# Performance work log

Hardware: AMD Instinct MI355X
Metric: run time of the kernel (lower is better)

## Reference

```python
import math
import jax, jax.numpy as jnp
import numpy as np

N_WIRES = 12
N_LAYERS = 3
BATCH = 2048
DIM = 2 ** N_WIRES


def _apply_1q(psi, U, wire):
    # psi: (B, 2^n) complex; U: (2,2) or (B,2,2)
    B = psi.shape[0]
    left = 2 ** wire
    psi = psi.reshape(B, left, 2, -1)
    if U.ndim == 3:
        psi = jnp.einsum('bij,bajc->baic', U, psi)
    else:
        psi = jnp.einsum('ij,bajc->baic', U, psi)
    return psi.reshape(B, -1)


def _apply_cnot(psi, wire):
    # CNOT on (control=wire, target=wire+1), adjacent wires
    B = psi.shape[0]
    left = 2 ** wire
    psi = psi.reshape(B, left, 2, 2, -1)
    flipped = psi[:, :, 1, ::-1, :][:, :, None]   # control=1 branch, target flipped
    psi = jnp.concatenate([psi[:, :, 0:1], flipped], axis=2)
    return psi.reshape(B, -1)


def _ry(theta):
    # RY(t) = [[cos t/2, -sin t/2],[sin t/2, cos t/2]]; theta: () or (B,)
    c = jnp.cos(theta / 2)
    s = jnp.sin(theta / 2)
    U = jnp.stack([jnp.stack([c, -s], -1), jnp.stack([s, c], -1)], -2)
    return U.astype(jnp.complex64)


def _rz(theta):
    # RZ(t) = diag(e^{-it/2}, e^{it/2}); theta scalar
    em = jnp.exp(-0.5j * theta.astype(jnp.complex64))
    ep = jnp.exp(0.5j * theta.astype(jnp.complex64))
    e00 = jnp.array([[1, 0], [0, 0]], dtype=jnp.complex64)
    e11 = jnp.array([[0, 0], [0, 1]], dtype=jnp.complex64)
    return e00 * em + e11 * ep


def _measure_z(psi):
    # <Z_w> for every wire; psi: (B, 2^n)
    B = psi.shape[0]
    p = jnp.abs(psi) ** 2
    outs = []
    for w in range(N_WIRES):
        pr = p.reshape(B, 2 ** w, 2, -1)
        outs.append(pr[:, :, 0].sum((1, 2)) - pr[:, :, 1].sum((1, 2)))
    return jnp.stack(outs, axis=-1)  # (B, n_wires)


def _forward(x, W1, b1, ry_theta, rz_theta, W2, b2):
    feat = x @ W1.T + b1                      # (B, n_wires)
    angles = jnp.tanh(feat) * math.pi         # encoding angles
    B = x.shape[0]
    psi = jnp.zeros((B, DIM), dtype=jnp.complex64).at[:, 0].set(1.0)
    # data encoding: per-sample RY on each wire
    for w in range(N_WIRES):
        psi = _apply_1q(psi, _ry(angles[:, w]), w)
    # variational layers with SHARED ry/rz params (module reuse in torch code)
    Ury = _ry(ry_theta)
    Urz = _rz(rz_theta)
    for _ in range(N_LAYERS):
        for w in range(N_WIRES):
            psi = _apply_1q(psi, Ury, w)
            psi = _apply_1q(psi, Urz, w)
        for w in range(N_WIRES - 1):
            psi = _apply_cnot(psi, w)
    z = _measure_z(psi)                        # (B, n_wires) real
    return z @ W2.T + b2                       # (B, 10) logits


def setup_inputs() -> dict:
    key = jax.random.key(0)
    ks = jax.random.split(key, 7)
    return {
        'x': jax.random.normal(ks[0], (BATCH, 784), dtype=jnp.float32),
        'W1': jax.random.normal(ks[1], (N_WIRES, 784), dtype=jnp.float32) * 0.03,
        'b1': jnp.zeros((N_WIRES,), dtype=jnp.float32),
        'ry_theta': jax.random.uniform(ks[2], (), dtype=jnp.float32) * 2 * math.pi,
        'rz_theta': jax.random.uniform(ks[3], (), dtype=jnp.float32) * 2 * math.pi,
        'W2': jax.random.normal(ks[4], (10, N_WIRES), dtype=jnp.float32) * 0.2,
        'b2': jnp.zeros((10,), dtype=jnp.float32),
    }


def reference(x, W1, b1, ry_theta, rz_theta, W2, b2):
    return _forward(x, W1, b1, ry_theta, rz_theta, W2, b2)
```

## Files before the change

### kernel.cpp

```cpp
#include <hip/hip_runtime.h>
#include <math.h>

#define NW   12
#define DIM  4096
#define TPB  256

typedef float v2f __attribute__((ext_vector_type(2)));

template<int CTRL>
__device__ __forceinline__ float fdpp(float v) {
    union { float f; int i; } u, w;
    u.f = v;
    w.i = __builtin_amdgcn_update_dpp(0, u.i, CTRL, 0xF, 0xF, false);
    return w.f;
}

template<int B>
__device__ __forceinline__ void ry_reg(v2f* r, float c, v2f vps, v2f vms) {
#pragma unroll
    for (int p = 0; p < 8; ++p) {
        const int i0 = ((p >> B) << (B + 1)) | (p & ((1 << B) - 1));
        const int i1 = i0 | (1 << B);
        const v2f a = r[i0], b = r[i1];
        r[i0] = __builtin_elementwise_fma(vms, b, a * c);
        r[i1] = __builtin_elementwise_fma(vps, a, b * c);
    }
}

template<int CTRL>
__device__ __forceinline__ void ry_dpp(v2f* r, float c, v2f vsp) {
#pragma unroll
    for (int k = 0; k < 16; ++k) {
        const v2f p = { fdpp<CTRL>(r[k].x), fdpp<CTRL>(r[k].y) };
        r[k] = __builtin_elementwise_fma(vsp, p, r[k] * c);
    }
}

__device__ __forceinline__ void ry_xor4(v2f* r, float c, v2f vsp) {
#pragma unroll
    for (int k = 0; k < 16; ++k) {
        const v2f p = { fdpp<0x141>(fdpp<0x1B>(r[k].x)),
                        fdpp<0x141>(fdpp<0x1B>(r[k].y)) };
        r[k] = __builtin_elementwise_fma(vsp, p, r[k] * c);
    }
}

__global__ __launch_bounds__(TPB, 4)
void qmnist_kernel(const float* __restrict__ x,  const float* __restrict__ W1,
                   const float* __restrict__ b1, const float* __restrict__ ryp,
                   const float* __restrict__ rzp, const float* __restrict__ W2,
                   const float* __restrict__ b2, float* __restrict__ out) {
    __shared__ v2f psi[DIM];
    float* smf  = (float*)psi;
    float* wred = smf;
    float* encc = smf + 48;
    float* encs = smf + 60;
    float* zfin = smf + 72;

    const int tid  = threadIdx.x;
    const int blk  = blockIdx.x;
    const int lane = tid & 63;
    const int wave = tid >> 6;

    float acc[NW];
#pragma unroll
    for (int w = 0; w < NW; ++w) acc[w] = 0.f;
    if (tid < 196) {
        const float4 xv = ((const float4*)(x + (size_t)blk * 784))[tid];
#pragma unroll
        for (int w = 0; w < NW; ++w) {
            const float4 wv = ((const float4*)(W1 + w * 784))[tid];
            acc[w] = fmaf(xv.x, wv.x, fmaf(xv.y, wv.y, fmaf(xv.z, wv.z, xv.w * wv.w)));
        }
    }
#pragma unroll
    for (int w = 0; w < NW; ++w) {
        float v = acc[w];
        v += __shfl_down(v, 32);
        v += __shfl_down(v, 16);
        v += __shfl_down(v, 8);
        v += __shfl_down(v, 4);
        v += __shfl_down(v, 2);
        v += __shfl_down(v, 1);
        if (lane == 0) wred[wave * NW + w] = v;
    }
    __syncthreads();
    if (tid < NW) {
        float feat = wred[tid] + wred[NW + tid] + wred[2 * NW + tid] + wred[3 * NW + tid] + b1[tid];
        float a = tanhf(feat) * 3.14159265358979323846f;
        float h = 0.5f * a;
        encc[tid] = cosf(h);
        encs[tid] = sinf(h);
    }
    __syncthreads();

    float hi = 1.f;
#pragma unroll
    for (int b = 0; b < 8; ++b)
        hi *= ((tid >> b) & 1) ? encs[11 - b] : encc[11 - b];
    v2f r[16];
#pragma unroll
    for (int k = 0; k < 16; ++k) {
        float f = hi;
        f *= (k & 1) ? encs[3] : encc[3];
        f *= (k & 2) ? encs[2] : encc[2];
        f *= (k & 4) ? encs[1] : encc[1];
        f *= (k & 8) ? encs[0] : encc[0];
        r[k] = (v2f){ f, 0.f };
    }

    const float ry = ryp[0], rz = rzp[0];
    const float c = cosf(0.5f * ry), s = sinf(0.5f * ry);
    const v2f vps = {  s,  s };
    const v2f vms = { -s, -s };
    const int pcT = __popc(tid);
    v2f qv[5], qp[5];
#pragma unroll
    for (int j = 0; j < 5; ++j) {
        const float ang = rz * (float)(pcT + j - 6);
        const float qc = cosf(ang), qs = sinf(ang);
        qv[j] = (v2f){  qc, qs };
        qp[j] = (v2f){ -qs, qc };
    }

    const v2f vs0 = (lane & 1) ? vps : vms;
    const v2f vs1 = (lane & 2) ? vps : vms;
    const v2f vs2 = (lane & 4) ? vps : vms;
    const v2f vs3 = (lane & 8) ? vps : vms;

    const int base_r = (tid & 15) | ((tid & 240) << 4);
    const int gt     = tid ^ (tid >> 1);

    for (int layer = 0; layer < 3; ++layer) {
        ry_reg<0>(r, c, vps, vms); ry_reg<1>(r, c, vps, vms);
        ry_reg<2>(r, c, vps, vms); ry_reg<3>(r, c, vps, vms);
        ry_dpp<0xB1>(r, c, vs0);
        ry_dpp<0x4E>(r, c, vs1);
        ry_xor4(r, c, vs2);
        ry_dpp<0x128>(r, c, vs3);

        __syncthreads();
#pragma unroll
        for (int k = 0; k < 16; ++k)
            psi[(k << 8) | tid] = r[k];
        __syncthreads();
#pragma unroll
        for (int k = 0; k < 16; ++k)
            r[k] = psi[base_r | (k << 4)];

        ry_reg<0>(r, c, vps, vms); ry_reg<1>(r, c, vps, vms);
        ry_reg<2>(r, c, vps, vms); ry_reg<3>(r, c, vps, vms);

#pragma unroll
        for (int k = 0; k < 16; ++k) {
            const int j = __popc(k);
            r[k] = __builtin_elementwise_fma((v2f){ r[k].y, r[k].y }, qp[j], qv[j] * r[k].x);
        }

#pragma unroll
        for (int k = 0; k < 16; ++k)
            psi[base_r | (k << 4)] = r[k];
        __syncthreads();
#pragma unroll
        for (int k = 0; k < 16; ++k) {
            const int gk = (k ^ (k >> 1)) & 15;
            r[k] = psi[(gt ^ ((k & 1) << 7)) | (gk << 8)];
        }
    }
    __syncthreads();

    float t_total = 0.f, s3 = 0.f, s2 = 0.f, s1 = 0.f, s0 = 0.f;
#pragma unroll
    for (int k = 0; k < 16; ++k) {
        const float pp = fmaf(r[k].x, r[k].x, r[k].y * r[k].y);
        t_total += pp;
        if (k & 1) s3 += pp;
        if (k & 2) s2 += pp;
        if (k & 4) s1 += pp;
        if (k & 8) s0 += pp;
    }
    float contrib[NW];
    contrib[3] = t_total - 2.f * s3;
    contrib[2] = t_total - 2.f * s2;
    contrib[1] = t_total - 2.f * s1;
    contrib[0] = t_total - 2.f * s0;
#pragma unroll
    for (int b = 0; b < 8; ++b) {
        const int w = 11 - b;
        contrib[w] = ((tid >> b) & 1) ? -t_total : t_total;
    }
#pragma unroll
    for (int w = 0; w < NW; ++w) {
        float v = contrib[w];
        v += __shfl_down(v, 32);
        v += __shfl_down(v, 16);
        v += __shfl_down(v, 8);
        v += __shfl_down(v, 4);
        v += __shfl_down(v, 2);
        v += __shfl_down(v, 1);
        if (lane == 0) wred[wave * NW + w] = v;
    }
    __syncthreads();
    if (tid < NW)
        zfin[tid] = wred[tid] + wred[NW + tid] + wred[2 * NW + tid] + wred[3 * NW + tid];
    __syncthreads();

    if (tid < 10) {
        float o = b2[tid];
#pragma unroll
        for (int w = 0; w < NW; ++w)
            o = fmaf(zfin[w], W2[tid * NW + w], o);
        out[(size_t)blk * 10 + tid] = o;
    }
}

extern "C" void kernel_launch(void* const* d_in, const int* in_sizes, int n_in,
                              void* d_out, int out_size, void* d_ws, size_t ws_size,
                              hipStream_t stream) {
    const float* x   = (const float*)d_in[0];
    const float* W1  = (const float*)d_in[1];
    const float* b1  = (const float*)d_in[2];
    const float* ry  = (const float*)d_in[3];
    const float* rz  = (const float*)d_in[4];
    const float* W2  = (const float*)d_in[5];
    const float* b2  = (const float*)d_in[6];
    float* out = (float*)d_out;

    const int batch = in_sizes[0] / 784;
    qmnist_kernel<<<batch, TPB, 0, stream>>>(x, W1, b1, ry, rz, W2, b2, out);
}
```

Before: 115.9 us.

## Drop final-layer RZ and CNOT pass, fold CNOT ladder into parity-based measurement

```diff
diff --git a/kernel.cpp b/kernel.cpp
--- a/kernel.cpp
+++ b/kernel.cpp
@@ -131,23 +131,25 @@
     const int base_r = (tid & 15) | ((tid & 240) << 4);
     const int gt     = tid ^ (tid >> 1);
 
-    for (int layer = 0; layer < 3; ++layer) {
+    for (int layer = 0; layer < 2; ++layer) {
+        __syncthreads();
+
         ry_reg<0>(r, c, vps, vms); ry_reg<1>(r, c, vps, vms);
         ry_reg<2>(r, c, vps, vms); ry_reg<3>(r, c, vps, vms);
+
+#pragma unroll
+        for (int k = 0; k < 16; ++k)
+            psi[(k << 8) | tid] = r[k];
+        __syncthreads();
+#pragma unroll
+        for (int k = 0; k < 16; ++k)
+            r[k] = psi[base_r | (k << 4)];
+
         ry_dpp<0xB1>(r, c, vs0);
         ry_dpp<0x4E>(r, c, vs1);
         ry_xor4(r, c, vs2);
         ry_dpp<0x128>(r, c, vs3);
 
-        __syncthreads();
-#pragma unroll
-        for (int k = 0; k < 16; ++k)
-            psi[(k << 8) | tid] = r[k];
-        __syncthreads();
-#pragma unroll
-        for (int k = 0; k < 16; ++k)
-            r[k] = psi[base_r | (k << 4)];
-
         ry_reg<0>(r, c, vps, vms); ry_reg<1>(r, c, vps, vms);
         ry_reg<2>(r, c, vps, vms); ry_reg<3>(r, c, vps, vms);
 
@@ -167,28 +169,52 @@
             r[k] = psi[(gt ^ ((k & 1) << 7)) | (gk << 8)];
         }
     }
-    __syncthreads();
-
-    float t_total = 0.f, s3 = 0.f, s2 = 0.f, s1 = 0.f, s0 = 0.f;
+
+    __syncthreads();
+    ry_reg<0>(r, c, vps, vms); ry_reg<1>(r, c, vps, vms);
+    ry_reg<2>(r, c, vps, vms); ry_reg<3>(r, c, vps, vms);
+#pragma unroll
+    for (int k = 0; k < 16; ++k)
+        psi[(k << 8) | tid] = r[k];
+    __syncthreads();
+#pragma unroll
+    for (int k = 0; k < 16; ++k)
+        r[k] = psi[base_r | (k << 4)];
+    ry_dpp<0xB1>(r, c, vs0);
+    ry_dpp<0x4E>(r, c, vs1);
+    ry_xor4(r, c, vs2);
+    ry_dpp<0x128>(r, c, vs3);
+    ry_reg<0>(r, c, vps, vms); ry_reg<1>(r, c, vps, vms);
+    ry_reg<2>(r, c, vps, vms); ry_reg<3>(r, c, vps, vms);
+    __syncthreads();
+
+    float T = 0.f, Sp = 0.f, S1 = 0.f, S2 = 0.f, S3 = 0.f;
 #pragma unroll
     for (int k = 0; k < 16; ++k) {
         const float pp = fmaf(r[k].x, r[k].x, r[k].y * r[k].y);
-        t_total += pp;
-        if (k & 1) s3 += pp;
-        if (k & 2) s2 += pp;
-        if (k & 4) s1 += pp;
-        if (k & 8) s0 += pp;
-    }
+        T += pp;
+        Sp += (__popc(k) & 1)        ? -pp : pp;
+        S1 += (__popc(k >> 1) & 1)   ? -pp : pp;
+        S2 += (__popc(k >> 2) & 1)   ? -pp : pp;
+        S3 += ((k >> 3) & 1)         ? -pp : pp;
+    }
+    const int t1 = (tid >> 1) & 1, t2 = (tid >> 2) & 1, t3 = (tid >> 3) & 1;
+    const int t4 = (tid >> 4) & 1, t5 = (tid >> 5) & 1, t6 = (tid >> 6) & 1,
+              t7 = (tid >> 7) & 1;
+    const int p47 = t4 ^ t5 ^ t6 ^ t7;
     float contrib[NW];
-    contrib[3] = t_total - 2.f * s3;
-    contrib[2] = t_total - 2.f * s2;
-    contrib[1] = t_total - 2.f * s1;
-    contrib[0] = t_total - 2.f * s0;
-#pragma unroll
-    for (int b = 0; b < 8; ++b) {
-        const int w = 11 - b;
-        contrib[w] = ((tid >> b) & 1) ? -t_total : t_total;
-    }
+    contrib[0]  = t7                  ? -T : T;
+    contrib[1]  = (t6 ^ t7)           ? -T : T;
+    contrib[2]  = (t5 ^ t6 ^ t7)      ? -T : T;
+    contrib[3]  = p47                 ? -T : T;
+    contrib[4]  = p47                 ? -S3 : S3;
+    contrib[5]  = p47                 ? -S2 : S2;
+    contrib[6]  = p47                 ? -S1 : S1;
+    contrib[7]  = p47                 ? -Sp : Sp;
+    contrib[8]  = (t3 ^ p47)          ? -Sp : Sp;
+    contrib[9]  = (t2 ^ t3 ^ p47)     ? -Sp : Sp;
+    contrib[10] = (t1 ^ t2 ^ t3 ^ p47) ? -Sp : Sp;
+    contrib[11] = (pcT & 1)           ? -Sp : Sp;
 #pragma unroll
     for (int w = 0; w < NW; ++w) {
         float v = contrib[w];
```

Result: no change. 115.6 us (-0.2%).

## Process two samples per block and interleave their gate stages across shared-memory exchanges

Applied to the files above, without the earlier changes.

```diff
diff --git a/kernel.cpp b/kernel.cpp
--- a/kernel.cpp
+++ b/kernel.cpp
@@ -15,6 +15,10 @@
     return w.f;
 }
 
+__device__ __forceinline__ v2f cmulq(v2f a, v2f b) {
+    return (v2f){ fmaf(a.x, b.x, -a.y * b.y), fmaf(a.x, b.y, a.y * b.x) };
+}
+
 template<int B>
 __device__ __forceinline__ void ry_reg(v2f* r, float c, v2f vps, v2f vms) {
 #pragma unroll
@@ -44,6 +48,48 @@
         r[k] = __builtin_elementwise_fma(vsp, p, r[k] * c);
     }
 }
+
+__device__ __forceinline__ void measure12(const v2f* r, int tid, float* contrib) {
+    float T = 0.f, Sp = 0.f, Sa = 0.f, Sb = 0.f, Sc = 0.f;
+#pragma unroll
+    for (int k = 0; k < 16; ++k) {
+        const float pp = fmaf(r[k].x, r[k].x, r[k].y * r[k].y);
+        T += pp;
+        Sp += (__popc(k) & 1)      ? -pp : pp;
+        Sa += (__popc(k >> 1) & 1) ? -pp : pp;
+        Sb += (__popc(k >> 2) & 1) ? -pp : pp;
+        Sc += ((k >> 3) & 1)       ? -pp : pp;
+    }
+    const int t1 = (tid >> 1) & 1, t2 = (tid >> 2) & 1, t3 = (tid >> 3) & 1;
+    const int t4 = (tid >> 4) & 1, t5 = (tid >> 5) & 1, t6 = (tid >> 6) & 1,
+              t7 = (tid >> 7) & 1;
+    const int p47 = t4 ^ t5 ^ t6 ^ t7;
+    contrib[0]  = t7                   ? -T : T;
+    contrib[1]  = (t6 ^ t7)            ? -T : T;
+    contrib[2]  = (t5 ^ t6 ^ t7)       ? -T : T;
+    contrib[3]  = p47                  ? -T : T;
+    contrib[4]  = p47                  ? -Sc : Sc;
+    contrib[5]  = p47                  ? -Sb : Sb;
+    contrib[6]  = p47                  ? -Sa : Sa;
+    contrib[7]  = p47                  ? -Sp : Sp;
+    contrib[8]  = (t3 ^ p47)           ? -Sp : Sp;
+    contrib[9]  = (t2 ^ t3 ^ p47)      ? -Sp : Sp;
+    contrib[10] = (t1 ^ t2 ^ t3 ^ p47) ? -Sp : Sp;
+    contrib[11] = (__popc(tid) & 1)    ? -Sp : Sp;
+}
+
+#define PW1(r) _Pragma("unroll") for (int k = 0; k < 16; ++k) psi[(k << 8) | tid] = (r)[k];
+#define PR1(r) _Pragma("unroll") for (int k = 0; k < 16; ++k) (r)[k] = psi[base_r | (k << 4)];
+#define PW2(r) _Pragma("unroll") for (int k = 0; k < 16; ++k) psi[base_r | (k << 4)] = (r)[k];
+#define PR2(r) _Pragma("unroll") for (int k = 0; k < 16; ++k) { \
+        const int gk = (k ^ (k >> 1)) & 15; \
+        (r)[k] = psi[(gt ^ ((k & 1) << 7)) | (gk << 8)]; }
+#define RZF(r) _Pragma("unroll") for (int k = 0; k < 16; ++k) { \
+        const int j = __popc(k); (r)[k] = cmulq((r)[k], qv[j]); }
+#define GREG(r) { ry_reg<0>(r, c, vps, vms); ry_reg<1>(r, c, vps, vms); \
+                  ry_reg<2>(r, c, vps, vms); ry_reg<3>(r, c, vps, vms); }
+#define GDPP(r) { ry_dpp<0xB1>(r, c, vs0); ry_dpp<0x4E>(r, c, vs1); \
+                  ry_xor4(r, c, vs2);      ry_dpp<0x128>(r, c, vs3); }
 
 __global__ __launch_bounds__(TPB, 4)
 void qmnist_kernel(const float* __restrict__ x,  const float* __restrict__ W1,
@@ -53,40 +99,43 @@
     __shared__ v2f psi[DIM];
     float* smf  = (float*)psi;
     float* wred = smf;
-    float* encc = smf + 48;
-    float* encs = smf + 60;
-    float* zfin = smf + 72;
+    float* encc = smf + 96;
+    float* encs = smf + 120;
+    float* zfin = smf + 144;
 
     const int tid  = threadIdx.x;
     const int blk  = blockIdx.x;
     const int lane = tid & 63;
     const int wave = tid >> 6;
 
-    float acc[NW];
-#pragma unroll
-    for (int w = 0; w < NW; ++w) acc[w] = 0.f;
+    float acc[2 * NW];
+#pragma unroll
+    for (int j = 0; j < 2 * NW; ++j) acc[j] = 0.f;
     if (tid < 196) {
-        const float4 xv = ((const float4*)(x + (size_t)blk * 784))[tid];
+        const float4 xv0 = ((const float4*)(x + (size_t)(2 * blk)     * 784))[tid];
+        const float4 xv1 = ((const float4*)(x + (size_t)(2 * blk + 1) * 784))[tid];
 #pragma unroll
         for (int w = 0; w < NW; ++w) {
             const float4 wv = ((const float4*)(W1 + w * 784))[tid];
-            acc[w] = fmaf(xv.x, wv.x, fmaf(xv.y, wv.y, fmaf(xv.z, wv.z, xv.w * wv.w)));
+            acc[w]      = fmaf(xv0.x, wv.x, fmaf(xv0.y, wv.y, fmaf(xv0.z, wv.z, xv0.w * wv.w)));
+            acc[NW + w] = fmaf(xv1.x, wv.x, fmaf(xv1.y, wv.y, fmaf(xv1.z, wv.z, xv1.w * wv.w)));
         }
     }
 #pragma unroll
-    for (int w = 0; w < NW; ++w) {
-        float v = acc[w];
+    for (int j = 0; j < 2 * NW; ++j) {
+        float v = acc[j];
         v += __shfl_down(v, 32);
         v += __shfl_down(v, 16);
         v += __shfl_down(v, 8);
         v += __shfl_down(v, 4);
         v += __shfl_down(v, 2);
         v += __shfl_down(v, 1);
-        if (lane == 0) wred[wave * NW + w] = v;
-    }
-    __syncthreads();
-    if (tid < NW) {
-        float feat = wred[tid] + wred[NW + tid] + wred[2 * NW + tid] + wred[3 * NW + tid] + b1[tid];
+        if (lane == 0) wred[wave * 24 + j] = v;
+    }
+    __syncthreads();
+    if (tid < 2 * NW) {
+        const int w = (tid >= NW) ? tid - NW : tid;
+        float feat = wred[tid] + wred[24 + tid] + wred[48 + tid] + wred[72 + tid] + b1[w];
         float a = tanhf(feat) * 3.14159265358979323846f;
         float h = 0.5f * a;
         encc[tid] = cosf(h);
@@ -94,19 +143,24 @@
     }
     __syncthreads();
 
-    float hi = 1.f;
-#pragma unroll
-    for (int b = 0; b < 8; ++b)
-        hi *= ((tid >> b) & 1) ? encs[11 - b] : encc[11 - b];
-    v2f r[16];
-#pragma unroll
-    for (int k = 0; k < 16; ++k) {
-        float f = hi;
-        f *= (k & 1) ? encs[3] : encc[3];
-        f *= (k & 2) ? encs[2] : encc[2];
-        f *= (k & 4) ? encs[1] : encc[1];
-        f *= (k & 8) ? encs[0] : encc[0];
-        r[k] = (v2f){ f, 0.f };
+    float hiA = 1.f, hiB = 1.f;
+#pragma unroll
+    for (int b = 0; b < 8; ++b) {
+        const int w = 11 - b;
+        const bool o = (tid >> b) & 1;
+        hiA *= o ? encs[w]      : encc[w];
+        hiB *= o ? encs[NW + w] : encc[NW + w];
+    }
+    v2f rA[16], rB[16];
+#pragma unroll
+    for (int k = 0; k < 16; ++k) {
+        float fA = hiA, fB = hiB;
+        fA *= (k & 1) ? encs[3] : encc[3];   fB *= (k & 1) ? encs[NW + 3] : encc[NW + 3];
+        fA *= (k & 2) ? encs[2] : encc[2];   fB *= (k & 2) ? encs[NW + 2] : encc[NW + 2];
+        fA *= (k & 4) ? encs[1] : encc[1];   fB *= (k & 4) ? encs[NW + 1] : encc[NW + 1];
+        fA *= (k & 8) ? encs[0] : encc[0];   fB *= (k & 8) ? encs[NW + 0] : encc[NW + 0];
+        rA[k] = (v2f){ fA, 0.f };
+        rB[k] = (v2f){ fB, 0.f };
     }
 
     const float ry = ryp[0], rz = rzp[0];
@@ -114,95 +168,76 @@
     const v2f vps = {  s,  s };
     const v2f vms = { -s, -s };
     const int pcT = __popc(tid);
-    v2f qv[5], qp[5];
-#pragma unroll
-    for (int j = 0; j < 5; ++j) {
-        const float ang = rz * (float)(pcT + j - 6);
-        const float qc = cosf(ang), qs = sinf(ang);
-        qv[j] = (v2f){  qc, qs };
-        qp[j] = (v2f){ -qs, qc };
-    }
-
+    v2f qv[5];
+    {
+        float sb, cb; __sincosf(rz * (float)(pcT - 6), &sb, &cb);
+        float sd, cd; __sincosf(rz, &sd, &cd);
+        qv[0] = (v2f){ cb, sb };
+        const v2f step = (v2f){ cd, sd };
+#pragma unroll
+        for (int j = 1; j < 5; ++j) qv[j] = cmulq(qv[j - 1], step);
+    }
     const v2f vs0 = (lane & 1) ? vps : vms;
     const v2f vs1 = (lane & 2) ? vps : vms;
     const v2f vs2 = (lane & 4) ? vps : vms;
     const v2f vs3 = (lane & 8) ? vps : vms;
-
     const int base_r = (tid & 15) | ((tid & 240) << 4);
     const int gt     = tid ^ (tid >> 1);
 
-    for (int layer = 0; layer < 3; ++layer) {
-        ry_reg<0>(r, c, vps, vms); ry_reg<1>(r, c, vps, vms);
-        ry_reg<2>(r, c, vps, vms); ry_reg<3>(r, c, vps, vms);
-        ry_dpp<0xB1>(r, c, vs0);
-        ry_dpp<0x4E>(r, c, vs1);
-        ry_xor4(r, c, vs2);
-        ry_dpp<0x128>(r, c, vs3);
-
-        __syncthreads();
-#pragma unroll
-        for (int k = 0; k < 16; ++k)
-            psi[(k << 8) | tid] = r[k];
-        __syncthreads();
-#pragma unroll
-        for (int k = 0; k < 16; ++k)
-            r[k] = psi[base_r | (k << 4)];
-
-        ry_reg<0>(r, c, vps, vms); ry_reg<1>(r, c, vps, vms);
-        ry_reg<2>(r, c, vps, vms); ry_reg<3>(r, c, vps, vms);
-
-#pragma unroll
-        for (int k = 0; k < 16; ++k) {
-            const int j = __popc(k);
-            r[k] = __builtin_elementwise_fma((v2f){ r[k].y, r[k].y }, qp[j], qv[j] * r[k].x);
+    GREG(rA); GDPP(rA);
+    __syncthreads();
+    for (int layer = 0; layer < 2; ++layer) {
+        PW1(rA); GREG(rB);
+        __syncthreads();
+        PR1(rA); GDPP(rB);
+        GREG(rA); RZF(rA);
+        PW2(rA);
+        __syncthreads();
+        PR2(rA);
+        __syncthreads();
+        PW1(rB); GREG(rA);
+        __syncthreads();
+        PR1(rB); GDPP(rA);
+        GREG(rB); RZF(rB);
+        PW2(rB);
+        __syncthreads();
+        PR2(rB);
+        __syncthreads();
+    }
+    PW1(rA); GREG(rB);
+    __syncthreads();
+    PR1(rA); GDPP(rB);
+    GREG(rA);
+    __syncthreads();
+    float cA[NW], cB[NW];
+    PW1(rB); measure12(rA, tid, cA);
+    __syncthreads();
+    PR1(rB);
+    GREG(rB);
+    __syncthreads();
+    measure12(rB, tid, cB);
+
+#pragma unroll
+    for (int w = 0; w < NW; ++w) {
+        float va = cA[w], vb = cB[w];
+        va += __shfl_down(va, 32);  vb += __shfl_down(vb, 32);
+        va += __shfl_down(va, 16);  vb += __shfl_down(vb, 16);
+        va += __shfl_down(va, 8);   vb += __shfl_down(vb, 8);
+        va += __shfl_down(va, 4);   vb += __shfl_down(vb, 4);
+        va += __shfl_down(va, 2);   vb += __shfl_down(vb, 2);
+        va += __shfl_down(va, 1);   vb += __shfl_down(vb, 1);
+        if (lane == 0) {
+            wred[wave * NW + w]      = va;
+            wred[48 + wave * NW + w] = vb;
         }
-
-#pragma unroll
-        for (int k = 0; k < 16; ++k)
-            psi[base_r | (k << 4)] = r[k];
-        __syncthreads();
-#pragma unroll
-        for (int k = 0; k < 16; ++k) {
-            const int gk = (k ^ (k >> 1)) & 15;
-            r[k] = psi[(gt ^ ((k & 1) << 7)) | (gk << 8)];
-        }
-    }
-    __syncthreads();
-
-    float t_total = 0.f, s3 = 0.f, s2 = 0.f, s1 = 0.f, s0 = 0.f;
-#pragma unroll
-    for (int k = 0; k < 16; ++k) {
-        const float pp = fmaf(r[k].x, r[k].x, r[k].y * r[k].y);
-        t_total += pp;
-        if (k & 1) s3 += pp;
-        if (k & 2) s2 += pp;
-        if (k & 4) s1 += pp;
-        if (k & 8) s0 += pp;
-    }
-    float contrib[NW];
-    contrib[3] = t_total - 2.f * s3;
-    contrib[2] = t_total - 2.f * s2;
-    contrib[1] = t_total - 2.f * s1;
-    contrib[0] = t_total - 2.f * s0;
-#pragma unroll
-    for (int b = 0; b < 8; ++b) {
-        const int w = 11 - b;
-        contrib[w] = ((tid >> b) & 1) ? -t_total : t_total;
-    }
-#pragma unroll
-    for (int w = 0; w < NW; ++w) {
-        float v = contrib[w];
-        v += __shfl_down(v, 32);
-        v += __shfl_down(v, 16);
-        v += __shfl_down(v, 8);
-        v += __shfl_down(v, 4);
-        v += __shfl_down(v, 2);
-        v += __shfl_down(v, 1);
-        if (lane == 0) wred[wave * NW + w] = v;
-    }
-    __syncthreads();
-    if (tid < NW)
-        zfin[tid] = wred[tid] + wred[NW + tid] + wred[2 * NW + tid] + wred[3 * NW + tid];
+    }
+    __syncthreads();
+    if (tid < 2 * NW) {
+        const int sm = (tid >= NW) ? 1 : 0;
+        const int w  = tid - sm * NW;
+        zfin[tid] = wred[48 * sm + w] + wred[48 * sm + NW + w]
+                  + wred[48 * sm + 2 * NW + w] + wred[48 * sm + 3 * NW + w];
+    }
     __syncthreads();
 
     if (tid < 10) {
@@ -210,7 +245,14 @@
 #pragma unroll
         for (int w = 0; w < NW; ++w)
             o = fmaf(zfin[w], W2[tid * NW + w], o);
-        out[(size_t)blk * 10 + tid] = o;
+        out[(size_t)(2 * blk) * 10 + tid] = o;
+    } else if (tid >= 64 && tid < 74) {
+        const int q = tid - 64;
+        float o = b2[q];
+#pragma unroll
+        for (int w = 0; w < NW; ++w)
+            o = fmaf(zfin[NW + w], W2[q * NW + w], o);
+        out[(size_t)(2 * blk + 1) * 10 + q] = o;
     }
 }
 
@@ -227,5 +269,5 @@
     float* out = (float*)d_out;
 
     const int batch = in_sizes[0] / 784;
-    qmnist_kernel<<<batch, TPB, 0, stream>>>(x, W1, b1, ry, rz, W2, b2, out);
-}
+    qmnist_kernel<<<batch / 2, TPB, 0, stream>>>(x, W1, b1, ry, rz, W2, b2, out);
+}
```

New measurement: 140.0 us. 1.21x slower.
